# Performance work log

Measured on AMD Instinct MI355X. Metric: run time of the kernel, lower is better.

## Reference

```python
import jax, jax.numpy as jnp
import numpy as np

M, H, D, P = 16, 32, 128, 8192
N = H * D


def setup_inputs() -> dict:
    key = jax.random.key(0)
    ks = jax.random.split(key, 8)
    w_scale = 0.3 / np.sqrt(N)  # keep q,k ~ N(0, 0.3^2) so exp(c) stays finite
    X = jax.random.normal(ks[0], (M, N), jnp.float32)
    Wq = jax.random.normal(ks[1], (N, N), jnp.float32) * w_scale
    Wk = jax.random.normal(ks[2], (N, N), jnp.float32) * w_scale
    Wv = jax.random.normal(ks[3], (N, N), jnp.float32) * w_scale
    cache_K = jax.random.normal(ks[4], (H, P, D), jnp.float32) * 0.3
    cache_V = jax.random.normal(ks[5], (H, P, D), jnp.float32) * 0.3
    tau = jnp.float32(2.0)
    noise = jax.random.normal(ks[6], (H, M, P + M), jnp.float32) * 0.1
    return {"X": X, "Wq": Wq, "Wk": Wk, "Wv": Wv,
            "cache_K": cache_K, "cache_V": cache_V, "tau": tau, "noise": noise}


def reference(X, Wq, Wk, Wv, cache_K, cache_V, tau, noise):
    h, p, d = cache_K.shape
    m, n = X.shape
    # RMS-style prenorm: X / sqrt(mean(X^2, dim=1))
    x_norm = X * jax.lax.rsqrt(jnp.sum(X * X, axis=1, keepdims=True) / n)
    # nn.Linear: y = x @ W^T; reshape to [H, M, D]
    q = (x_norm @ Wq.T).reshape(m, h, d).transpose(1, 0, 2)
    k = (x_norm @ Wk.T).reshape(m, h, d).transpose(1, 0, 2)
    v = (x_norm @ Wv.T).reshape(m, h, d).transpose(1, 0, 2)
    k_cache = jnp.concatenate([cache_K, k], axis=1)  # [H, P+M, D]
    v_cache = jnp.concatenate([cache_V, v], axis=1)
    c = jnp.einsum('hmd,hpd->hmp', q, k_cache)  # [H, M, P+M]
    c_exp = jnp.exp(c)
    c_exp_perturb = jnp.exp((c + noise) / tau)
    c_div = c_exp / jnp.sum(c_exp, axis=2, keepdims=True)
    c_div_perturb = c_exp_perturb / jnp.sum(c_exp_perturb, axis=2, keepdims=True)
    c_out = jnp.sum(c_div_perturb, axis=1)  # [H, P+M]
    o = jnp.einsum('hmp,hpd->hmd', c_div, v_cache)  # [H, M, D]
    o2 = o.transpose(1, 0, 2).reshape(m, n)
    return o2, c_out
```

## Files before the change

### kernel.cpp

```cpp
#include <hip/hip_runtime.h>

#define M_ 16
#define H_ 32
#define D_ 128
#define P_ 8192
#define N_ 4096
#define PM_ 8208

#define WS_Q    0
#define WS_K    65536
#define WS_V    131072
#define WS_S1   196608
#define WS_S2   197120
#define WS_IS2  197632
#define WS_XQ   198144
#define WS_E2   263680
#define WS_PP   263680
#define WS_PO   4466176
#define WS_SP1  6563328
#define WS_SP2  6579712

typedef __attribute__((address_space(1))) const void gvoid_t;
typedef __attribute__((address_space(3))) void lvoid_t;

__global__ __launch_bounds__(256) void rmsnorm_kernel(const float* __restrict__ X,
                                                      float* __restrict__ ws) {
  int m = blockIdx.x, t = threadIdx.x;
  __shared__ float red[256];
  const float4* X4 = (const float4*)(X + (size_t)m * N_);
  float s = 0.f;
  #pragma unroll
  for (int q = 0; q < 4; q++) {
    float4 v = X4[t + q * 256];
    s += v.x * v.x + v.y * v.y + v.z * v.z + v.w * v.w;
  }
  red[t] = s;
  __syncthreads();
  for (int off = 128; off > 0; off >>= 1) {
    if (t < off) red[t] += red[t + off];
    __syncthreads();
  }
  float scale = rsqrtf(red[0] * (1.0f / N_));
  float4* xq = (float4*)(ws + WS_XQ);
  #pragma unroll
  for (int q = 0; q < 4; q++) {
    int nq = t + q * 256;
    float4 v = X4[nq];
    v.x *= scale; v.y *= scale; v.z *= scale; v.w *= scale;
    xq[nq * 16 + m] = v;
  }
}

__global__ __launch_bounds__(256, 4) void proj_kernel(const float* __restrict__ Wq,
                                                      const float* __restrict__ Wk,
                                                      const float* __restrict__ Wv,
                                                      const float* __restrict__ xr,
                                                      float* __restrict__ ws) {
  __shared__ float tile[4 * 2048];
  int widx = threadIdx.x >> 6, lane = threadIdx.x & 63;
  int kc = blockIdx.x / 48;
  int jt = (blockIdx.x % 48) * 4 + widx;
  int jj0 = jt * 64;
  int sel = jj0 >> 12;
  int j0 = jj0 & 4095;
  const float* Wm = (sel == 0) ? Wq : ((sel == 1) ? Wk : Wv);
  int n0 = kc * 256;

  float* tl = tile + widx * 2048;
  int g8 = lane >> 3;
  int c8 = lane & 7;
  int cq = c8 ^ g8;

  const float* gsrc[8];
  #pragma unroll
  for (int i = 0; i < 8; i++)
    gsrc[i] = Wm + (size_t)(j0 + i * 8 + g8) * N_ + n0 + cq * 4;

  const float4* tl4 = (const float4*)tl;
  int rbase = lane * 8;
  int swz = lane & 7;

  const float4* xr4 = (const float4*)xr;
  float acc[16];
  #pragma unroll
  for (int m = 0; m < 16; m++) acc[m] = 0.f;

  for (int ti = 0; ti < 8; ti++) {
    #pragma unroll
    for (int i = 0; i < 8; i++)
      __builtin_amdgcn_global_load_lds((gvoid_t*)(gsrc[i] + ti * 32),
                                       (lvoid_t*)(tl + i * 256), 16, 0, 0);
    asm volatile("s_waitcnt vmcnt(0)" ::: "memory");
    __builtin_amdgcn_sched_barrier(0);

    int nqb = (n0 >> 2) + ti * 8;
    #pragma unroll
    for (int k = 0; k < 8; k++) {
      float4 w4 = tl4[rbase + (k ^ swz)];
      int qbase = (nqb + k) * 16;
      #pragma unroll
      for (int m = 0; m < 16; m++) {
        float4 xm = xr4[qbase + m];
        acc[m] += xm.x * w4.x + xm.y * w4.y + xm.z * w4.z + xm.w * w4.w;
      }
    }
  }

  float* pp = ws + WS_PP + (size_t)kc * 16 * 12288 + jj0 + lane;
  #pragma unroll
  for (int m = 0; m < 16; m++) pp[(size_t)m * 12288] = acc[m];
}

__global__ __launch_bounds__(256) void proj_reduce_kernel(float* __restrict__ ws) {
  int tid = blockIdx.x * 256 + threadIdx.x;
  int m = tid / 12288;
  int j = tid - m * 12288;
  float acc = 0.f;
  #pragma unroll
  for (int kc = 0; kc < 16; kc++)
    acc += ws[WS_PP + ((size_t)(kc * 16 + m)) * 12288 + j];
  int sel = j >> 12, jj = j & 4095;
  int h = jj >> 7, d = jj & 127;
  ws[WS_Q + sel * 65536 + (h * 16 + m) * 128 + d] = acc;
}

__global__ __launch_bounds__(256) void attn_kernel(const float* __restrict__ cacheK,
                                                   const float* __restrict__ cacheV,
                                                   const float* __restrict__ noise,
                                                   const float* __restrict__ taup,
                                                   float* __restrict__ ws) {
  __shared__ float red[4 * 2048];
  __shared__ float sred[2][4][16];
  int h = blockIdx.x >> 5, b = blockIdx.x & 31;
  int widx = threadIdx.x >> 6, lane = threadIdx.x & 63;
  int m8 = lane & 7, sl = lane >> 3;
  int rsel = lane >> 4;
  int msel = lane & 15;
  bool tb = (lane >> 3) & 1;
  bool rb0 = rsel & 1, rb1 = (rsel >> 1) & 1;
  float inv_tau = 1.0f / taup[0];

  float qv[2][16];
  #pragma unroll
  for (int t = 0; t < 2; t++) {
    const float4* qp = (const float4*)(ws + WS_Q + ((size_t)(h * 16) + m8 + 8 * t) * 128 + sl * 16);
    #pragma unroll
    for (int jq = 0; jq < 4; jq++) {
      float4 v = qp[jq];
      qv[t][jq * 4] = v.x; qv[t][jq * 4 + 1] = v.y;
      qv[t][jq * 4 + 2] = v.z; qv[t][jq * 4 + 3] = v.w;
    }
  }
  float oacc[2][16];
  #pragma unroll
  for (int t = 0; t < 2; t++)
    #pragma unroll
    for (int j = 0; j < 16; j++) oacc[t][j] = 0.f;
  float s1 = 0.f, s2 = 0.f;

  const float* nbase = noise + ((size_t)h * 16 + msel) * PM_;
  float* e2base = ws + WS_E2 + (size_t)h * PM_ * 16 + msel;
  const float* kc_base = cacheK + (size_t)h * P_ * D_;
  const float* vc_base = cacheV + (size_t)h * P_ * D_;
  const float* kn_base = ws + WS_K + (size_t)h * 16 * 128;
  const float* vn_base = ws + WS_V + (size_t)h * 16 * 128;

  int g0 = b * 64;
  int gN = (b == 31) ? 68 : 64;
  for (int gl = widx; gl < gN; gl += 4) {
    int p0 = (g0 + gl) * 4;
    const float *kb, *vb;
    if (p0 < P_) { kb = kc_base + (size_t)p0 * D_; vb = vc_base + (size_t)p0 * D_; }
    else { kb = kn_base + (size_t)(p0 - P_) * D_; vb = vn_base + (size_t)(p0 - P_) * D_; }

    float nz = nbase[p0 + rsel];

    float pr[4][2];
    #pragma unroll
    for (int r = 0; r < 4; r++) {
      float4 kq[4];
      const float4* krp = (const float4*)(kb + r * D_ + sl * 16);
      kq[0] = krp[0]; kq[1] = krp[1]; kq[2] = krp[2]; kq[3] = krp[3];
      const float* kk = (const float*)kq;
      float t0 = 0.f, t1 = 0.f;
      #pragma unroll
      for (int j = 0; j < 16; j++) { t0 += kk[j] * qv[0][j]; t1 += kk[j] * qv[1][j]; }
      pr[r][0] = t0; pr[r][1] = t1;
    }
    float cc[4][2];
    #pragma unroll
    for (int r = 0; r < 4; r++)
      #pragma unroll
      for (int t = 0; t < 2; t++) {
        float v = pr[r][t];
        v += __shfl_xor(v, 8, 64);
        v += __shfl_xor(v, 16, 64);
        v += __shfl_xor(v, 32, 64);
        cc[r][t] = v;
      }

    float a0 = tb ? cc[0][1] : cc[0][0];
    float a1 = tb ? cc[1][1] : cc[1][0];
    float a2 = tb ? cc[2][1] : cc[2][0];
    float a3 = tb ? cc[3][1] : cc[3][0];
    float b0 = rb0 ? a1 : a0;
    float b1 = rb0 ? a3 : a2;
    float myc = rb1 ? b1 : b0;

    float e2 = __expf((myc + nz) * inv_tau);
    e2base[(size_t)(p0 + rsel) * 16] = e2;
    s2 += e2;

    float e1[4][2];
    #pragma unroll
    for (int r = 0; r < 4; r++) {
      e1[r][0] = __expf(cc[r][0]);
      e1[r][1] = __expf(cc[r][1]);
    }
    float f0 = tb ? e1[0][1] : e1[0][0];
    float f1 = tb ? e1[1][1] : e1[1][0];
    float f2 = tb ? e1[2][1] : e1[2][0];
    float f3 = tb ? e1[3][1] : e1[3][0];
    float g0s = rb0 ? f1 : f0;
    float g1s = rb0 ? f3 : f2;
    s1 += rb1 ? g1s : g0s;

    #pragma unroll
    for (int r = 0; r < 4; r++) {
      float4 vq[4];
      const float4* vrp = (const float4*)(vb + r * D_ + sl * 16);
      vq[0] = vrp[0]; vq[1] = vrp[1]; vq[2] = vrp[2]; vq[3] = vrp[3];
      const float* vv = (const float*)vq;
      float ea = e1[r][0], eb = e1[r][1];
      #pragma unroll
      for (int j = 0; j < 16; j++) {
        oacc[0][j] += ea * vv[j];
        oacc[1][j] += eb * vv[j];
      }
    }
  }

  s1 += __shfl_xor(s1, 16, 64); s1 += __shfl_xor(s1, 32, 64);
  s2 += __shfl_xor(s2, 16, 64); s2 += __shfl_xor(s2, 32, 64);
  if (lane < 16) { sred[0][widx][lane] = s1; sred[1][widx][lane] = s2; }

  float* rw = red + widx * 2048 + lane * 32;
  #pragma unroll
  for (int t = 0; t < 2; t++)
    #pragma unroll
    for (int j = 0; j < 16; j++) {
      int i = t * 16 + j;
      rw[(i + lane) & 31] = oacc[t][j];
    }
  __syncthreads();

  float* po = ws + WS_PO + (size_t)(h * 32 + b) * 2048;
  for (int e = threadIdx.x; e < 2048; e += 256) {
    int ln = e >> 5, i = e & 31;
    int phys = (ln << 5) + ((i + ln) & 31);
    float v = red[phys] + red[phys + 2048] + red[phys + 4096] + red[phys + 6144];
    int mo = (ln & 7) + 8 * (i >> 4);
    int d = (ln >> 3) * 16 + (i & 15);
    po[mo * 128 + d] = v;
  }
  if (threadIdx.x < 16) {
    int mm = threadIdx.x;
    float a  = sred[0][0][mm] + sred[0][1][mm] + sred[0][2][mm] + sred[0][3][mm];
    float c2 = sred[1][0][mm] + sred[1][1][mm] + sred[1][2][mm] + sred[1][3][mm];
    ws[WS_SP1 + (size_t)(h * 32 + b) * 16 + mm] = a;
    ws[WS_SP2 + (size_t)(h * 32 + b) * 16 + mm] = c2;
  }
}

__global__ __launch_bounds__(256) void sums_kernel(float* __restrict__ ws) {
  int tid = blockIdx.x * 256 + threadIdx.x;
  if (tid >= 512) return;
  int h = tid >> 4, m = tid & 15;
  float a = 0.f, c2 = 0.f;
  #pragma unroll
  for (int b = 0; b < 32; b++) {
    a  += ws[WS_SP1 + (size_t)(h * 32 + b) * 16 + m];
    c2 += ws[WS_SP2 + (size_t)(h * 32 + b) * 16 + m];
  }
  ws[WS_S1 + tid] = a;
  ws[WS_S2 + tid] = c2;
  ws[WS_IS2 + tid] = 1.0f / c2;
}

__global__ __launch_bounds__(256) void epilogue_kernel(const float* __restrict__ ws,
                                                       float* __restrict__ out) {
  int tid = blockIdx.x * 256 + threadIdx.x;
  int mm = tid >> 12, j = tid & 4095;
  int h = j >> 7, d = j & 127;
  float acc = 0.f;
  #pragma unroll
  for (int b = 0; b < 32; b++)
    acc += ws[WS_PO + (size_t)(h * 32 + b) * 2048 + mm * 128 + d];
  out[tid] = acc / ws[WS_S1 + h * 16 + mm];
}

__global__ __launch_bounds__(256) void cout_kernel(const float* __restrict__ ws,
                                                   float* __restrict__ out) {
  int tid = blockIdx.x * 256 + threadIdx.x;
  if (tid >= H_ * PM_) return;
  int h = tid / PM_, p = tid - h * PM_;
  const float4* e2p = (const float4*)(ws + WS_E2 + ((size_t)h * PM_ + p) * 16);
  const float* is2 = ws + WS_IS2 + h * 16;
  float acc = 0.f;
  #pragma unroll
  for (int q = 0; q < 4; q++) {
    float4 v = e2p[q];
    acc += v.x * is2[q * 4] + v.y * is2[q * 4 + 1] + v.z * is2[q * 4 + 2] + v.w * is2[q * 4 + 3];
  }
  out[65536 + tid] = acc;
}

extern "C" void kernel_launch(void* const* d_in, const int* in_sizes, int n_in,
                              void* d_out, int out_size, void* d_ws, size_t ws_size,
                              hipStream_t stream) {
  const float* X     = (const float*)d_in[0];
  const float* Wq    = (const float*)d_in[1];
  const float* Wk    = (const float*)d_in[2];
  const float* Wv    = (const float*)d_in[3];
  const float* cK    = (const float*)d_in[4];
  const float* cV    = (const float*)d_in[5];
  const float* tau   = (const float*)d_in[6];
  const float* noise = (const float*)d_in[7];
  float* out = (float*)d_out;
  float* ws  = (float*)d_ws;

  rmsnorm_kernel<<<16, 256, 0, stream>>>(X, ws);
  proj_kernel<<<768, 256, 0, stream>>>(Wq, Wk, Wv, ws + WS_XQ, ws);
  proj_reduce_kernel<<<768, 256, 0, stream>>>(ws);
  attn_kernel<<<1024, 256, 0, stream>>>(cK, cV, noise, tau, ws);
  sums_kernel<<<2, 256, 0, stream>>>(ws);
  epilogue_kernel<<<256, 256, 0, stream>>>(ws, out);
  cout_kernel<<<1026, 256, 0, stream>>>(ws, out);
}
```

Before: 215.5 us.

## Pre-transpose noise into E2 layout, unroll attention loop by two, drop block reduction

A new kernel transposes the noise tensor into the [P+M,16] workspace layout, so the attention kernel reads noise with coalesced loads from the same slot it later overwrites with e2. The attention loop now handles two groups per iteration to raise memory-level parallelism on the K and V loads. Per-warp partial sums go straight to global memory, and the sums kernel reduces 128 entries instead of 32, which removes the shared-memory reduction. This adds a kernel launch and a full extra pass over the noise data, plus higher register pressure in the attention kernel.

```diff
diff --git a/kernel.cpp b/kernel.cpp
--- a/kernel.cpp
+++ b/kernel.cpp
@@ -18,7 +18,7 @@
 #define WS_PP   263680
 #define WS_PO   4466176
 #define WS_SP1  6563328
-#define WS_SP2  6579712
+#define WS_SP2  6628864
 
 typedef __attribute__((address_space(1))) const void gvoid_t;
 typedef __attribute__((address_space(3))) void lvoid_t;
@@ -67,8 +67,7 @@
   int n0 = kc * 256;
 
   float* tl = tile + widx * 2048;
-  int g8 = lane >> 3;
-  int c8 = lane & 7;
+  int g8 = lane >> 3, c8 = lane & 7;
   int cq = c8 ^ g8;
 
   const float* gsrc[8];
@@ -124,18 +123,39 @@
   ws[WS_Q + sel * 65536 + (h * 16 + m) * 128 + d] = acc;
 }
 
+__global__ __launch_bounds__(256) void noise_t_kernel(const float* __restrict__ noise,
+                                                      float* __restrict__ ws) {
+  __shared__ float tile[16 * 68];
+  int blk = blockIdx.x;
+  int h = blk / 129, ct = blk % 129;
+  int c0 = ct * 64;
+  int t = threadIdx.x;
+  int rw = t >> 6, cc = t & 63;
+  #pragma unroll
+  for (int i = 0; i < 4; i++) {
+    int m = i * 4 + rw;
+    int c = c0 + cc;
+    if (c < PM_) tile[m * 68 + cc] = noise[((size_t)h * 16 + m) * PM_ + c];
+  }
+  __syncthreads();
+  float* outh = ws + WS_E2 + (size_t)h * PM_ * 16;
+  #pragma unroll
+  for (int i = 0; i < 4; i++) {
+    int flat = i * 256 + t;
+    int c = flat >> 4, m = flat & 15;
+    if (c0 + c < PM_) outh[(size_t)(c0 + c) * 16 + m] = tile[m * 68 + c];
+  }
+}
+
 __global__ __launch_bounds__(256) void attn_kernel(const float* __restrict__ cacheK,
                                                    const float* __restrict__ cacheV,
-                                                   const float* __restrict__ noise,
                                                    const float* __restrict__ taup,
                                                    float* __restrict__ ws) {
   __shared__ float red[4 * 2048];
-  __shared__ float sred[2][4][16];
   int h = blockIdx.x >> 5, b = blockIdx.x & 31;
   int widx = threadIdx.x >> 6, lane = threadIdx.x & 63;
   int m8 = lane & 7, sl = lane >> 3;
   int rsel = lane >> 4;
-  int msel = lane & 15;
   bool tb = (lane >> 3) & 1;
   bool rb0 = rsel & 1, rb1 = (rsel >> 1) & 1;
   float inv_tau = 1.0f / taup[0];
@@ -158,24 +178,17 @@
     for (int j = 0; j < 16; j++) oacc[t][j] = 0.f;
   float s1 = 0.f, s2 = 0.f;
 
-  const float* nbase = noise + ((size_t)h * 16 + msel) * PM_;
-  float* e2base = ws + WS_E2 + (size_t)h * PM_ * 16 + msel;
+  float* e2g = ws + WS_E2 + (size_t)h * PM_ * 16 + lane;
   const float* kc_base = cacheK + (size_t)h * P_ * D_;
   const float* vc_base = cacheV + (size_t)h * P_ * D_;
   const float* kn_base = ws + WS_K + (size_t)h * 16 * 128;
   const float* vn_base = ws + WS_V + (size_t)h * 16 * 128;
 
-  int g0 = b * 64;
-  int gN = (b == 31) ? 68 : 64;
-  for (int gl = widx; gl < gN; gl += 4) {
-    int p0 = (g0 + gl) * 4;
-    const float *kb, *vb;
+  auto kvp = [&](int p0, const float*& kb, const float*& vb) {
     if (p0 < P_) { kb = kc_base + (size_t)p0 * D_; vb = vc_base + (size_t)p0 * D_; }
     else { kb = kn_base + (size_t)(p0 - P_) * D_; vb = vn_base + (size_t)(p0 - P_) * D_; }
-
-    float nz = nbase[p0 + rsel];
-
-    float pr[4][2];
+  };
+  auto dotrows = [&](const float* kb, float (&pr)[4][2]) {
     #pragma unroll
     for (int r = 0; r < 4; r++) {
       float4 kq[4];
@@ -187,6 +200,8 @@
       for (int j = 0; j < 16; j++) { t0 += kk[j] * qv[0][j]; t1 += kk[j] * qv[1][j]; }
       pr[r][0] = t0; pr[r][1] = t1;
     }
+  };
+  auto finish = [&](float (&pr)[4][2], float nz, int p0, const float* vb) {
     float cc[4][2];
     #pragma unroll
     for (int r = 0; r < 4; r++)
@@ -198,7 +213,6 @@
         v += __shfl_xor(v, 32, 64);
         cc[r][t] = v;
       }
-
     float a0 = tb ? cc[0][1] : cc[0][0];
     float a1 = tb ? cc[1][1] : cc[1][0];
     float a2 = tb ? cc[2][1] : cc[2][0];
@@ -208,7 +222,7 @@
     float myc = rb1 ? b1 : b0;
 
     float e2 = __expf((myc + nz) * inv_tau);
-    e2base[(size_t)(p0 + rsel) * 16] = e2;
+    e2g[(size_t)p0 * 16] = e2;
     s2 += e2;
 
     float e1[4][2];
@@ -238,11 +252,41 @@
         oacc[1][j] += eb * vv[j];
       }
     }
+  };
+
+  int g0 = b * 64;
+  int gN = (b == 31) ? 68 : 64;
+  int gl = widx;
+  for (; gl + 4 < gN; gl += 8) {
+    int pA = (g0 + gl) * 4, pB = (g0 + gl + 4) * 4;
+    const float *kbA, *vbA, *kbB, *vbB;
+    kvp(pA, kbA, vbA);
+    kvp(pB, kbB, vbB);
+    float nzA = e2g[(size_t)pA * 16];
+    float nzB = e2g[(size_t)pB * 16];
+    float prA[4][2], prB[4][2];
+    dotrows(kbA, prA);
+    dotrows(kbB, prB);
+    finish(prA, nzA, pA, vbA);
+    finish(prB, nzB, pB, vbB);
+  }
+  if (gl < gN) {
+    int pA = (g0 + gl) * 4;
+    const float *kbA, *vbA;
+    kvp(pA, kbA, vbA);
+    float nzA = e2g[(size_t)pA * 16];
+    float prA[4][2];
+    dotrows(kbA, prA);
+    finish(prA, nzA, pA, vbA);
   }
 
   s1 += __shfl_xor(s1, 16, 64); s1 += __shfl_xor(s1, 32, 64);
   s2 += __shfl_xor(s2, 16, 64); s2 += __shfl_xor(s2, 32, 64);
-  if (lane < 16) { sred[0][widx][lane] = s1; sred[1][widx][lane] = s2; }
+  if (lane < 16) {
+    size_t sp = ((size_t)h * 128 + b * 4 + widx) * 16 + lane;
+    ws[WS_SP1 + sp] = s1;
+    ws[WS_SP2 + sp] = s2;
+  }
 
   float* rw = red + widx * 2048 + lane * 32;
   #pragma unroll
@@ -263,13 +307,6 @@
     int d = (ln >> 3) * 16 + (i & 15);
     po[mo * 128 + d] = v;
   }
-  if (threadIdx.x < 16) {
-    int mm = threadIdx.x;
-    float a  = sred[0][0][mm] + sred[0][1][mm] + sred[0][2][mm] + sred[0][3][mm];
-    float c2 = sred[1][0][mm] + sred[1][1][mm] + sred[1][2][mm] + sred[1][3][mm];
-    ws[WS_SP1 + (size_t)(h * 32 + b) * 16 + mm] = a;
-    ws[WS_SP2 + (size_t)(h * 32 + b) * 16 + mm] = c2;
-  }
 }
 
 __global__ __launch_bounds__(256) void sums_kernel(float* __restrict__ ws) {
@@ -277,10 +314,9 @@
   if (tid >= 512) return;
   int h = tid >> 4, m = tid & 15;
   float a = 0.f, c2 = 0.f;
-  #pragma unroll
-  for (int b = 0; b < 32; b++) {
-    a  += ws[WS_SP1 + (size_t)(h * 32 + b) * 16 + m];
-    c2 += ws[WS_SP2 + (size_t)(h * 32 + b) * 16 + m];
+  for (int i = 0; i < 128; i++) {
+    a  += ws[WS_SP1 + ((size_t)h * 128 + i) * 16 + m];
+    c2 += ws[WS_SP2 + ((size_t)h * 128 + i) * 16 + m];
   }
   ws[WS_S1 + tid] = a;
   ws[WS_S2 + tid] = c2;
@@ -332,7 +368,8 @@
   rmsnorm_kernel<<<16, 256, 0, stream>>>(X, ws);
   proj_kernel<<<768, 256, 0, stream>>>(Wq, Wk, Wv, ws + WS_XQ, ws);
   proj_reduce_kernel<<<768, 256, 0, stream>>>(ws);
-  attn_kernel<<<1024, 256, 0, stream>>>(cK, cV, noise, tau, ws);
+  noise_t_kernel<<<32 * 129, 256, 0, stream>>>(noise, ws);
+  attn_kernel<<<1024, 256, 0, stream>>>(cK, cV, tau, ws);
   sums_kernel<<<2, 256, 0, stream>>>(ws);
   epilogue_kernel<<<256, 256, 0, stream>>>(ws, out);
   cout_kernel<<<1026, 256, 0, stream>>>(ws, out);
```

After: 259.6 us. 20.5% more time.

## Split attention into separate QK and PV kernels and double projection split-K

Applied to the files above, without the earlier changes.

The fused attention kernel is split into a QK kernel that computes scores, writes exp(c) values to a new workspace buffer and accumulates the row sums, and a PV kernel that reads those weights back and accumulates against V. The goal is to lower register pressure and raise occupancy in each pass. The cost is an extra launch plus a round trip of the 16x8208x32 exp matrix through global memory. Separately, the projection split-K factor goes from 16 to 32 chunks, doubling the block count, so the reduce kernel now has twice as many partial sums to add.

```diff
diff --git a/kernel.cpp b/kernel.cpp
--- a/kernel.cpp
+++ b/kernel.cpp
@@ -15,10 +15,11 @@
 #define WS_IS2  197632
 #define WS_XQ   198144
 #define WS_E2   263680
+#define WS_E1   4466176
 #define WS_PP   263680
-#define WS_PO   4466176
-#define WS_SP1  6563328
-#define WS_SP2  6579712
+#define WS_PO   8668672
+#define WS_SP1  10765824
+#define WS_SP2  10782208
 
 typedef __attribute__((address_space(1))) const void gvoid_t;
 typedef __attribute__((address_space(3))) void lvoid_t;
@@ -64,11 +65,10 @@
   int sel = jj0 >> 12;
   int j0 = jj0 & 4095;
   const float* Wm = (sel == 0) ? Wq : ((sel == 1) ? Wk : Wv);
-  int n0 = kc * 256;
+  int n0 = kc * 128;
 
   float* tl = tile + widx * 2048;
-  int g8 = lane >> 3;
-  int c8 = lane & 7;
+  int g8 = lane >> 3, c8 = lane & 7;
   int cq = c8 ^ g8;
 
   const float* gsrc[8];
@@ -85,7 +85,7 @@
   #pragma unroll
   for (int m = 0; m < 16; m++) acc[m] = 0.f;
 
-  for (int ti = 0; ti < 8; ti++) {
+  for (int ti = 0; ti < 4; ti++) {
     #pragma unroll
     for (int i = 0; i < 8; i++)
       __builtin_amdgcn_global_load_lds((gvoid_t*)(gsrc[i] + ti * 32),
@@ -117,19 +117,17 @@
   int j = tid - m * 12288;
   float acc = 0.f;
   #pragma unroll
-  for (int kc = 0; kc < 16; kc++)
+  for (int kc = 0; kc < 32; kc++)
     acc += ws[WS_PP + ((size_t)(kc * 16 + m)) * 12288 + j];
   int sel = j >> 12, jj = j & 4095;
   int h = jj >> 7, d = jj & 127;
   ws[WS_Q + sel * 65536 + (h * 16 + m) * 128 + d] = acc;
 }
 
-__global__ __launch_bounds__(256) void attn_kernel(const float* __restrict__ cacheK,
-                                                   const float* __restrict__ cacheV,
-                                                   const float* __restrict__ noise,
-                                                   const float* __restrict__ taup,
-                                                   float* __restrict__ ws) {
-  __shared__ float red[4 * 2048];
+__global__ __launch_bounds__(256) void qk_kernel(const float* __restrict__ cacheK,
+                                                 const float* __restrict__ noise,
+                                                 const float* __restrict__ taup,
+                                                 float* __restrict__ ws) {
   __shared__ float sred[2][4][16];
   int h = blockIdx.x >> 5, b = blockIdx.x & 31;
   int widx = threadIdx.x >> 6, lane = threadIdx.x & 63;
@@ -138,6 +136,7 @@
   int msel = lane & 15;
   bool tb = (lane >> 3) & 1;
   bool rb0 = rsel & 1, rb1 = (rsel >> 1) & 1;
+  bool hb = sl >> 2, sb0 = sl & 1, sb1 = (sl >> 1) & 1;
   float inv_tau = 1.0f / taup[0];
 
   float qv[2][16];
@@ -151,28 +150,14 @@
       qv[t][jq * 4 + 2] = v.z; qv[t][jq * 4 + 3] = v.w;
     }
   }
-  float oacc[2][16];
-  #pragma unroll
-  for (int t = 0; t < 2; t++)
-    #pragma unroll
-    for (int j = 0; j < 16; j++) oacc[t][j] = 0.f;
   float s1 = 0.f, s2 = 0.f;
 
   const float* nbase = noise + ((size_t)h * 16 + msel) * PM_;
   float* e2base = ws + WS_E2 + (size_t)h * PM_ * 16 + msel;
+  float* e1base = ws + WS_E1 + (size_t)h * PM_ * 16 + (sl & 3) * 16 + (sl >> 2) * 8 + m8;
   const float* kc_base = cacheK + (size_t)h * P_ * D_;
-  const float* vc_base = cacheV + (size_t)h * P_ * D_;
-  const float* kn_base = ws + WS_K + (size_t)h * 16 * 128;
-  const float* vn_base = ws + WS_V + (size_t)h * 16 * 128;
-
-  int g0 = b * 64;
-  int gN = (b == 31) ? 68 : 64;
-  for (int gl = widx; gl < gN; gl += 4) {
-    int p0 = (g0 + gl) * 4;
-    const float *kb, *vb;
-    if (p0 < P_) { kb = kc_base + (size_t)p0 * D_; vb = vc_base + (size_t)p0 * D_; }
-    else { kb = kn_base + (size_t)(p0 - P_) * D_; vb = vn_base + (size_t)(p0 - P_) * D_; }
-
+
+  auto qk_one = [&](int p0, const float* kb) {
     float nz = nbase[p0 + rsel];
 
     float pr[4][2];
@@ -206,7 +191,6 @@
     float b0 = rb0 ? a1 : a0;
     float b1 = rb0 ? a3 : a2;
     float myc = rb1 ? b1 : b0;
-
     float e2 = __expf((myc + nz) * inv_tau);
     e2base[(size_t)(p0 + rsel) * 16] = e2;
     s2 += e2;
@@ -225,24 +209,86 @@
     float g1s = rb0 ? f3 : f2;
     s1 += rb1 ? g1s : g0s;
 
+    float u0 = hb ? e1[0][1] : e1[0][0];
+    float u1 = hb ? e1[1][1] : e1[1][0];
+    float u2 = hb ? e1[2][1] : e1[2][0];
+    float u3 = hb ? e1[3][1] : e1[3][0];
+    float w0 = sb0 ? u1 : u0;
+    float w1 = sb0 ? u3 : u2;
+    float val = sb1 ? w1 : w0;
+    e1base[(size_t)p0 * 16] = val;
+  };
+
+  int g0 = b * 64;
+  for (int gl = widx; gl < 64; gl += 4) {
+    int p0 = (g0 + gl) * 4;
+    qk_one(p0, kc_base + (size_t)p0 * D_);
+  }
+  if (b == 31) {
+    int p0 = P_ + widx * 4;
+    qk_one(p0, ws + WS_K + ((size_t)h * 16 + widx * 4) * 128);
+  }
+
+  s1 += __shfl_xor(s1, 16, 64); s1 += __shfl_xor(s1, 32, 64);
+  s2 += __shfl_xor(s2, 16, 64); s2 += __shfl_xor(s2, 32, 64);
+  if (lane < 16) { sred[0][widx][lane] = s1; sred[1][widx][lane] = s2; }
+  __syncthreads();
+  if (threadIdx.x < 16) {
+    int mm = threadIdx.x;
+    float a  = sred[0][0][mm] + sred[0][1][mm] + sred[0][2][mm] + sred[0][3][mm];
+    float c2 = sred[1][0][mm] + sred[1][1][mm] + sred[1][2][mm] + sred[1][3][mm];
+    ws[WS_SP1 + (size_t)(h * 32 + b) * 16 + mm] = a;
+    ws[WS_SP2 + (size_t)(h * 32 + b) * 16 + mm] = c2;
+  }
+}
+
+__global__ __launch_bounds__(256) void pv_kernel(const float* __restrict__ cacheV,
+                                                 const float* __restrict__ ws,
+                                                 float* __restrict__ wout) {
+  __shared__ float red[4 * 2048];
+  int h = blockIdx.x >> 5, b = blockIdx.x & 31;
+  int widx = threadIdx.x >> 6, lane = threadIdx.x & 63;
+  int m8 = lane & 7, sl = lane >> 3;
+
+  float oacc[2][16];
+  #pragma unroll
+  for (int t = 0; t < 2; t++)
+    #pragma unroll
+    for (int j = 0; j < 16; j++) oacc[t][j] = 0.f;
+
+  const float* e1r = ws + WS_E1 + (size_t)h * PM_ * 16 + m8;
+  const float* vc_base = cacheV + (size_t)h * P_ * D_;
+
+  auto pv_one = [&](int p0, const float* vb) {
+    float ea[4], eb[4];
+    #pragma unroll
+    for (int r = 0; r < 4; r++) {
+      ea[r] = e1r[(size_t)p0 * 16 + r * 16];
+      eb[r] = e1r[(size_t)p0 * 16 + r * 16 + 8];
+    }
     #pragma unroll
     for (int r = 0; r < 4; r++) {
       float4 vq[4];
       const float4* vrp = (const float4*)(vb + r * D_ + sl * 16);
       vq[0] = vrp[0]; vq[1] = vrp[1]; vq[2] = vrp[2]; vq[3] = vrp[3];
       const float* vv = (const float*)vq;
-      float ea = e1[r][0], eb = e1[r][1];
       #pragma unroll
       for (int j = 0; j < 16; j++) {
-        oacc[0][j] += ea * vv[j];
-        oacc[1][j] += eb * vv[j];
+        oacc[0][j] += ea[r] * vv[j];
+        oacc[1][j] += eb[r] * vv[j];
       }
     }
-  }
-
-  s1 += __shfl_xor(s1, 16, 64); s1 += __shfl_xor(s1, 32, 64);
-  s2 += __shfl_xor(s2, 16, 64); s2 += __shfl_xor(s2, 32, 64);
-  if (lane < 16) { sred[0][widx][lane] = s1; sred[1][widx][lane] = s2; }
+  };
+
+  int g0 = b * 64;
+  for (int gl = widx; gl < 64; gl += 4) {
+    int p0 = (g0 + gl) * 4;
+    pv_one(p0, vc_base + (size_t)p0 * D_);
+  }
+  if (b == 31) {
+    int p0 = P_ + widx * 4;
+    pv_one(p0, ws + WS_V + ((size_t)h * 16 + widx * 4) * 128);
+  }
 
   float* rw = red + widx * 2048 + lane * 32;
   #pragma unroll
@@ -254,7 +300,7 @@
     }
   __syncthreads();
 
-  float* po = ws + WS_PO + (size_t)(h * 32 + b) * 2048;
+  float* po = wout + WS_PO + (size_t)(h * 32 + b) * 2048;
   for (int e = threadIdx.x; e < 2048; e += 256) {
     int ln = e >> 5, i = e & 31;
     int phys = (ln << 5) + ((i + ln) & 31);
@@ -262,13 +308,6 @@
     int mo = (ln & 7) + 8 * (i >> 4);
     int d = (ln >> 3) * 16 + (i & 15);
     po[mo * 128 + d] = v;
-  }
-  if (threadIdx.x < 16) {
-    int mm = threadIdx.x;
-    float a  = sred[0][0][mm] + sred[0][1][mm] + sred[0][2][mm] + sred[0][3][mm];
-    float c2 = sred[1][0][mm] + sred[1][1][mm] + sred[1][2][mm] + sred[1][3][mm];
-    ws[WS_SP1 + (size_t)(h * 32 + b) * 16 + mm] = a;
-    ws[WS_SP2 + (size_t)(h * 32 + b) * 16 + mm] = c2;
   }
 }
 
@@ -330,10 +369,11 @@
   float* ws  = (float*)d_ws;
 
   rmsnorm_kernel<<<16, 256, 0, stream>>>(X, ws);
-  proj_kernel<<<768, 256, 0, stream>>>(Wq, Wk, Wv, ws + WS_XQ, ws);
+  proj_kernel<<<1536, 256, 0, stream>>>(Wq, Wk, Wv, ws + WS_XQ, ws);
   proj_reduce_kernel<<<768, 256, 0, stream>>>(ws);
-  attn_kernel<<<1024, 256, 0, stream>>>(cK, cV, noise, tau, ws);
+  qk_kernel<<<1024, 256, 0, stream>>>(cK, noise, tau, ws);
   sums_kernel<<<2, 256, 0, stream>>>(ws);
+  pv_kernel<<<1024, 256, 0, stream>>>(cV, ws, ws);
   epilogue_kernel<<<256, 256, 0, stream>>>(ws, out);
   cout_kernel<<<1026, 256, 0, stream>>>(ws, out);
 }
```

New measurement: 226.3 us. +5.0%, slower.
